# Optimization experiments

Hardware: AMD Instinct MI355X
Metric: run time of the kernel (lower is better)

The kernel has to match this reference:

```python
import jax, jax.numpy as jnp
import numpy as np

B, C, H, W = 1, 256, 96, 96
C8 = C // 8
N = H * W


def setup_inputs() -> dict:
    key = jax.random.key(0)
    ks = jax.random.split(key, 12)
    inp = {
        "x": jax.random.normal(ks[0], (B, C, H, W), jnp.float32),
        "x_encoder": jax.random.normal(ks[1], (B, C, H, W), jnp.float32),
        # 1x1 conv params (weight stored as [out, in] matrices)
        "q_w": jax.random.normal(ks[2], (C8, C), jnp.float32) * 0.05,
        "q_b": jax.random.normal(ks[3], (C8,), jnp.float32) * 0.05,
        "k_w": jax.random.normal(ks[4], (C8, C), jnp.float32) * 0.05,
        "k_b": jax.random.normal(ks[5], (C8,), jnp.float32) * 0.05,
        "v_w": jax.random.normal(ks[6], (C, C), jnp.float32) * 0.05,
        "v_b": jax.random.normal(ks[7], (C,), jnp.float32) * 0.05,
        # positional bias parameters
        "h_pos": jax.random.normal(ks[8], (1, C8, H, 1), jnp.float32),
        "w_pos": jax.random.normal(ks[9], (1, C8, 1, W), jnp.float32),
        # gamma is zero-init in the module; use a random scalar for a non-trivial test
        "gamma": jax.random.normal(ks[10], (1,), jnp.float32),
    }
    return inp


def reference(x, x_encoder, q_w, q_b, k_w, k_b, v_w, v_b, h_pos, w_pos, gamma):
    b, c, h, w = x.shape
    n = h * w
    c8 = q_w.shape[0]
    # 1x1 convs == per-pixel linear maps
    query = (jnp.einsum('bchw,oc->bohw', x, q_w) + q_b[None, :, None, None])
    query = query.reshape(b, c8, n).transpose(0, 2, 1)            # [B, N, C8]
    key = (jnp.einsum('bchw,oc->bohw', x_encoder, k_w) + k_b[None, :, None, None])
    key = key.reshape(b, c8, n)                                   # [B, C8, N]
    # positional bias: broadcast-add then flatten, same as (height+width).view
    pos = (h_pos + w_pos).reshape(1, c8, n)                       # [1, C8, N]
    # energy = Q K^T + Q pos  ==  Q (K + pos)
    energy = jnp.einsum('bnc,bcm->bnm', query, key + pos)         # [B, N, N]
    attention = jax.nn.softmax(energy, axis=-1)
    value = (jnp.einsum('bchw,oc->bohw', x_encoder, v_w) + v_b[None, :, None, None])
    value = value.reshape(b, c, n)                                # [B, C, N]
    out = jnp.einsum('bcm,bnm->bcn', value, attention)            # [B, C, N]
    out = out.reshape(b, c, w, h)  # matches torch .view(B, C, W, H)
    return gamma * out + x
```

## Files before the change

### kernel.cpp

```cpp
#include <hip/hip_runtime.h>
#include <hip/hip_bf16.h>

#define NN 9216
#define CC 256
#define LOG2E 1.4426950408889634f

typedef __attribute__((ext_vector_type(8))) short short8;
typedef __attribute__((ext_vector_type(16))) float floatx16;
typedef __attribute__((ext_vector_type(4))) float floatx4;
typedef __attribute__((ext_vector_type(4))) unsigned short ushortx4;

#if __has_builtin(__builtin_amdgcn_exp2f)
#define fexp2 __builtin_amdgcn_exp2f
#else
#define fexp2 exp2f
#endif

__device__ __forceinline__ unsigned short f2bf(float f) {
    unsigned u = __float_as_uint(f);
    u = u + 0x7fffu + ((u >> 16) & 1u);
    return (unsigned short)(u >> 16);
}
__device__ __forceinline__ float bf2f(unsigned short s) {
    return __uint_as_float(((unsigned)s) << 16);
}
__device__ __forceinline__ unsigned pack2bf(float a, float b) {
    union { __hip_bfloat162 h; unsigned u; } cv;
    cv.h = __float22bfloat162_rn(make_float2(a, b));
    return cv.u;
}
__device__ __forceinline__ floatx16 mfma_bf16(short8 a, short8 b, floatx16 c) {
    return __builtin_amdgcn_mfma_f32_32x32x16_bf16(a, b, c, 0, 0, 0);
}

__global__ __launch_bounds__(256) void prep(
    const float* __restrict__ x, const float* __restrict__ xe,
    short* __restrict__ XBhi, short* __restrict__ XBlo,
    short* __restrict__ EBhi, short* __restrict__ EBlo)
{
    int t = threadIdx.x;
    const float* in = blockIdx.y ? xe : x;
    short* Dhi = blockIdx.y ? EBhi : XBhi;
    short* Dlo = blockIdx.y ? EBlo : XBlo;
    int tl = t & 31, sub = t >> 5;
    int nt = blockIdx.x >> 2, q4 = blockIdx.x & 3;
    int sub2 = q4 * 8 + sub;
    int kb_ = sub2 >> 1, hl = sub2 & 1;
    int n = nt * 32 + tl;
    int c0 = kb_ * 16 + hl * 8;
    union { unsigned short us[8]; short8 v8; } hi, lo;
#pragma unroll
    for (int j = 0; j < 8; ++j) {
        float val = in[(size_t)(c0 + j) * NN + n];
        unsigned short hb = f2bf(val);
        hi.us[j] = hb;
        lo.us[j] = f2bf(val - bf2f(hb));
    }
    size_t off = (((size_t)nt * 16 + kb_) * 64 + hl * 32 + tl) * 8;
    *(short8*)(Dhi + off) = hi.v8;
    *(short8*)(Dlo + off) = lo.v8;
}

__global__ __launch_bounds__(256) void wprep(
    const float* __restrict__ qw, const float* __restrict__ kw,
    const float* __restrict__ vw,
    short* __restrict__ WAhi, short* __restrict__ WAlo)
{
    int g = blockIdx.x * 256 + threadIdx.x;
    int lane = g & 63, kb_ = (g >> 6) & 15, ot = g >> 10;
    int o = lane & 31, half = lane >> 5;
    int c0 = kb_ * 16 + half * 8;
    const float* wsrc;
    int orow;
    float scale = 1.f;
    if (ot == 0) { wsrc = qw; orow = o; scale = LOG2E; }
    else if (ot == 1) { wsrc = kw; orow = o; }
    else { wsrc = vw; orow = (ot - 2) * 32 + o; }
    union { unsigned short us[8]; short8 v8; } hi, lo;
#pragma unroll
    for (int j = 0; j < 8; ++j) {
        float val = wsrc[(size_t)orow * 256 + c0 + j] * scale;
        unsigned short hb = f2bf(val);
        hi.us[j] = hb;
        lo.us[j] = f2bf(val - bf2f(hb));
    }
    size_t off = (((size_t)ot * 16 + kb_) * 64 + lane) * 8;
    *(short8*)(WAhi + off) = hi.v8;
    *(short8*)(WAlo + off) = lo.v8;
}

__global__ __launch_bounds__(256) void gemm_all(
    const short* __restrict__ XBhi, const short* __restrict__ XBlo,
    const short* __restrict__ EBhi, const short* __restrict__ EBlo,
    const short* __restrict__ WAhi, const short* __restrict__ WAlo,
    const float* __restrict__ qb, const float* __restrict__ kb,
    const float* __restrict__ hpos, const float* __restrict__ wpos,
    const float* __restrict__ vb,
    short* __restrict__ Qhi, short* __restrict__ Qlo,
    short* __restrict__ KP2, short* __restrict__ VF)
{
    __shared__ float lds[4][1024];
    int t = threadIdx.x;
    int wv = t >> 6, lane = t & 63, ln = lane & 31, h = lane >> 5;
    int nt = blockIdx.x * 2 + (wv & 1);
    int tile = blockIdx.y * 2 + (wv >> 1);

    const short* Bhi = (tile == 0 ? XBhi : EBhi) + (size_t)nt * 8192 + lane * 8;
    const short* Blo = (tile == 0 ? XBlo : EBlo) + (size_t)nt * 8192 + lane * 8;
    const short* Ahi = WAhi + (size_t)tile * 8192 + lane * 8;
    const short* Alo = WAlo + (size_t)tile * 8192 + lane * 8;

    floatx16 D;
#pragma unroll
    for (int r = 0; r < 16; ++r) D[r] = 0.f;
#pragma unroll
    for (int k = 0; k < 16; ++k) {
        short8 bh = *(const short8*)(Bhi + k * 512);
        short8 bl = *(const short8*)(Blo + k * 512);
        short8 ah = *(const short8*)(Ahi + k * 512);
        short8 al = *(const short8*)(Alo + k * 512);
        D = mfma_bf16(ah, bh, D);
        D = mfma_bf16(ah, bl, D);
        D = mfma_bf16(al, bh, D);
    }

    float* L = lds[wv];
#pragma unroll
    for (int r = 0; r < 16; ++r) {
        int row = (r & 3) + 8 * (r >> 2) + 4 * h;
        L[row * 32 + ((ln + row) & 31)] = D[r];
    }
    __syncthreads();

    if (tile == 0) {
        int n = nt * 32 + ln;
#pragma unroll
        for (int it = 0; it < 2; ++it) {
            int j0 = it * 16 + h * 8;
            union { unsigned short us[8]; short8 v8; } qh_, ql_;
#pragma unroll
            for (int jj = 0; jj < 8; ++jj) {
                int row = j0 + jj;
                float d = L[row * 32 + ((ln + row) & 31)] + qb[row] * LOG2E;
                unsigned short hb = f2bf(d);
                qh_.us[jj] = hb;
                ql_.us[jj] = f2bf(d - bf2f(hb));
            }
            *(short8*)(Qhi + (size_t)n * 32 + j0) = qh_.v8;
            *(short8*)(Qlo + (size_t)n * 32 + j0) = ql_.v8;
        }
    } else if (tile == 1) {
        int n = nt * 32 + ln;
        int hh = ((n >> 5) * 683) >> 11;
        int ww = n - hh * 96;
#pragma unroll
        for (int it = 0; it < 2; ++it) {
            int jb0 = it * 16 + h * 8;
            union { unsigned short us[8]; short8 v8; } o;
#pragma unroll
            for (int jj = 0; jj < 8; ++jj) {
                int row = jb0 + jj;
                float d = L[row * 32 + ((ln + row) & 31)]
                        + kb[row] + hpos[row * 96 + hh] + wpos[row * 96 + ww];
                o.us[jj] = f2bf(d);
            }
            *(short8*)(KP2 + (size_t)nt * 1024 + it * 512 + h * 256 + ln * 8) = o.v8;
        }
    } else {
        int cc = tile - 2;
        float bias = vb[cc * 32 + ln];
#pragma unroll
        for (int it = 0; it < 2; ++it) {
            union { unsigned short us[8]; short8 v8; } o;
#pragma unroll
            for (int ee = 0; ee < 8; ++ee) {
                int ml = it * 16 + h * 8 + ee;
                float d = L[ln * 32 + ((ml + ln) & 31)];
                o.us[ee] = f2bf(d + bias);
            }
            *(short8*)(VF + ((size_t)(nt * 2 + it) * 8 + cc) * 512 + lane * 8) = o.v8;
        }
    }
}

#define FSTEP(AH0, AH1, M0) do {                                                      \
    const size_t mo_ = (size_t)(M0) * 256;                                            \
    short8 va0 = *(const short8*)(Vb + mo_);                                          \
    short8 va1 = *(const short8*)(Vb + mo_ + 512);                                    \
    short8 va2 = *(const short8*)(Vb + mo_ + 1024);                                   \
    short8 va3 = *(const short8*)(Vb + mo_ + 1536);                                   \
    floatx16 S = {0.f,0.f,0.f,0.f,0.f,0.f,0.f,0.f,0.f,0.f,0.f,0.f,0.f,0.f,0.f,0.f};  \
    S = mfma_bf16(AH0, qf00, S);                                                      \
    S = mfma_bf16(AH0, qf01, S);                                                      \
    S = mfma_bf16(AH1, qf10, S);                                                      \
    S = mfma_bf16(AH1, qf11, S);                                                      \
    short8 va4 = *(const short8*)(Vb + mo_ + 2048);                                   \
    short8 va5 = *(const short8*)(Vb + mo_ + 2560);                                   \
    short8 va6 = *(const short8*)(Vb + mo_ + 3072);                                   \
    short8 va7 = *(const short8*)(Vb + mo_ + 3584);                                   \
    float ps = 0.f;                                                                   \
    _Pragma("unroll") for (int r = 0; r < 16; ++r) { S[r] = fexp2(S[r]); ps += S[r]; } \
    ps += __shfl_xor(ps, 32); l_run += ps;                                            \
    unsigned w0 = pack2bf(S[0], S[1]),  w1 = pack2bf(S[2], S[3]);                     \
    unsigned w2 = pack2bf(S[4], S[5]),  w3 = pack2bf(S[6], S[7]);                     \
    unsigned w4 = pack2bf(S[8], S[9]),  w5 = pack2bf(S[10], S[11]);                   \
    unsigned w6 = pack2bf(S[12], S[13]), w7 = pack2bf(S[14], S[15]);                  \
    {   unsigned p0 = h ? w0 : w2, p1 = h ? w1 : w3;                                  \
        unsigned e0 = (unsigned)__shfl_xor((int)p0, 32);                              \
        unsigned e1 = (unsigned)__shfl_xor((int)p1, 32);                              \
        union { unsigned u[4]; short8 v; } pf;                                        \
        pf.u[0] = h ? e0 : w0; pf.u[1] = h ? e1 : w1;                                 \
        pf.u[2] = h ? w2 : e0; pf.u[3] = h ? w3 : e1;                                 \
        O0 = mfma_bf16(va0, pf.v, O0); O1 = mfma_bf16(va1, pf.v, O1);                 \
        O2 = mfma_bf16(va2, pf.v, O2); O3 = mfma_bf16(va3, pf.v, O3);                 \
        O4 = mfma_bf16(va4, pf.v, O4); O5 = mfma_bf16(va5, pf.v, O5);                 \
        O6 = mfma_bf16(va6, pf.v, O6); O7 = mfma_bf16(va7, pf.v, O7); }               \
    short8 vb0 = *(const short8*)(Vb + mo_ + 4096);                                   \
    short8 vb1 = *(const short8*)(Vb + mo_ + 4608);                                   \
    short8 vb2 = *(const short8*)(Vb + mo_ + 5120);                                   \
    short8 vb3 = *(const short8*)(Vb + mo_ + 5632);                                   \
    short8 vb4 = *(const short8*)(Vb + mo_ + 6144);                                   \
    short8 vb5 = *(const short8*)(Vb + mo_ + 6656);                                   \
    short8 vb6 = *(const short8*)(Vb + mo_ + 7168);                                   \
    short8 vb7 = *(const short8*)(Vb + mo_ + 7680);                                   \
    {   unsigned p0 = h ? w4 : w6, p1 = h ? w5 : w7;                                  \
        unsigned e0 = (unsigned)__shfl_xor((int)p0, 32);                              \
        unsigned e1 = (unsigned)__shfl_xor((int)p1, 32);                              \
        union { unsigned u[4]; short8 v; } pf;                                        \
        pf.u[0] = h ? e0 : w4; pf.u[1] = h ? e1 : w5;                                 \
        pf.u[2] = h ? w6 : e0; pf.u[3] = h ? w7 : e1;                                 \
        O0 = mfma_bf16(vb0, pf.v, O0); O1 = mfma_bf16(vb1, pf.v, O1);                 \
        O2 = mfma_bf16(vb2, pf.v, O2); O3 = mfma_bf16(vb3, pf.v, O3);                 \
        O4 = mfma_bf16(vb4, pf.v, O4); O5 = mfma_bf16(vb5, pf.v, O5);                 \
        O6 = mfma_bf16(vb6, pf.v, O6); O7 = mfma_bf16(vb7, pf.v, O7); }               \
} while (0)

#define OGW(G, OG) { _Pragma("unroll") for (int r = 0; r < 16; ++r) { \
    int row = 32*(G) + (r & 3) + 8*(r >> 2) + 4*h;                    \
    Opart[obase + (size_t)row * NN + n0 + ln] = f2bf(OG[r]); } }

__global__ __launch_bounds__(128, 2) void flash(
    const short* __restrict__ Qhi, const short* __restrict__ Qlo,
    const short* __restrict__ KP2, const short* __restrict__ VT2,
    unsigned short* __restrict__ Opart, float* __restrict__ Lpart)
{
    int t = threadIdx.x;
    int wv = t >> 6;
    int lane = t & 63;
    int ln = lane & 31;
    int h = lane >> 5;
    int nt = blockIdx.x >> 2, mq = blockIdx.x & 3;
    int n0 = nt * 64 + wv * 32;
    int mstart = mq * 2304;

    int qoff = (n0 + ln) * 32 + h * 8;
    short8 qf00 = *(const short8*)(Qhi + qoff);
    short8 qf10 = *(const short8*)(Qhi + qoff + 16);
    short8 qf01 = *(const short8*)(Qlo + qoff);
    short8 qf11 = *(const short8*)(Qlo + qoff + 16);

    const short* Vb  = VT2 + (size_t)mstart * 256 + (size_t)lane * 8;
    const short* KPb = KP2 + (size_t)mstart * 32 + (size_t)lane * 8;

    floatx16 O0, O1, O2, O3, O4, O5, O6, O7;
#pragma unroll
    for (int r = 0; r < 16; ++r) {
        O0[r] = 0.f; O1[r] = 0.f; O2[r] = 0.f; O3[r] = 0.f;
        O4[r] = 0.f; O5[r] = 0.f; O6[r] = 0.f; O7[r] = 0.f;
    }
    float l_run = 0.f;

    short8 ahA0 = *(const short8*)(KPb);
    short8 ahA1 = *(const short8*)(KPb + 512);
    short8 ahB0, ahB1;

    for (int sp = 0; sp < 36; ++sp) {
        int m0 = sp * 64;
        ahB0 = *(const short8*)(KPb + (size_t)(m0 + 32) * 32);
        ahB1 = *(const short8*)(KPb + (size_t)(m0 + 32) * 32 + 512);
        FSTEP(ahA0, ahA1, m0);
        int nm = (sp < 35) ? (m0 + 64) : 0;
        ahA0 = *(const short8*)(KPb + (size_t)nm * 32);
        ahA1 = *(const short8*)(KPb + (size_t)nm * 32 + 512);
        FSTEP(ahB0, ahB1, m0 + 32);
    }

    if (lane < 32) Lpart[mq * NN + n0 + ln] = l_run;
    size_t obase = (size_t)mq * ((size_t)CC * NN);
    OGW(0,O0) OGW(1,O1) OGW(2,O2) OGW(3,O3) OGW(4,O4) OGW(5,O5) OGW(6,O6) OGW(7,O7)
}

__global__ __launch_bounds__(256) void stats(
    const float* __restrict__ Lpart, const float* __restrict__ gamma,
    float* __restrict__ W)
{
    int n = blockIdx.x * 256 + threadIdx.x;
    float L = Lpart[n] + Lpart[NN + n] + Lpart[2 * NN + n] + Lpart[3 * NN + n];
    W[n] = gamma[0] / L;
}

__global__ __launch_bounds__(256) void combine(
    const unsigned short* __restrict__ Opart, const float* __restrict__ W,
    const float* __restrict__ x, float* __restrict__ out)
{
    int i = blockIdx.x * 256 + threadIdx.x;
    int flat = i * 4;
    int n = flat % NN;
    floatx4 acc = *(const floatx4*)&x[flat];
    floatx4 w = *(const floatx4*)&W[n];
    float s0 = 0.f, s1 = 0.f, s2 = 0.f, s3 = 0.f;
#pragma unroll
    for (int q = 0; q < 4; ++q) {
        ushortx4 o = *(const ushortx4*)(Opart + (size_t)q * ((size_t)CC * NN) + flat);
        s0 += bf2f(o[0]); s1 += bf2f(o[1]); s2 += bf2f(o[2]); s3 += bf2f(o[3]);
    }
    acc[0] += s0 * w[0]; acc[1] += s1 * w[1]; acc[2] += s2 * w[2]; acc[3] += s3 * w[3];
    *(floatx4*)&out[flat] = acc;
}

extern "C" void kernel_launch(void* const* d_in, const int* in_sizes, int n_in,
                              void* d_out, int out_size, void* d_ws, size_t ws_size,
                              hipStream_t stream) {
    const float* x  = (const float*)d_in[0];
    const float* xe = (const float*)d_in[1];
    const float* qw = (const float*)d_in[2];
    const float* qb = (const float*)d_in[3];
    const float* kw = (const float*)d_in[4];
    const float* kb = (const float*)d_in[5];
    const float* vw = (const float*)d_in[6];
    const float* vb = (const float*)d_in[7];
    const float* hp = (const float*)d_in[8];
    const float* wp = (const float*)d_in[9];
    const float* gm = (const float*)d_in[10];

    char* ws = (char*)d_ws;
    short* Qhi  = (short*)(ws + 0);
    short* Qlo  = (short*)(ws + 589824);
    short* KP2  = (short*)(ws + 1179648);
    short* WAhi = (short*)(ws + 1769472);
    short* WAlo = (short*)(ws + 1933312);
    short* VF   = (short*)(ws + 2097152);
    unsigned short* Opart = (unsigned short*)(ws + 6815744);
    short* XBhi = (short*)(ws + 6815744);
    short* XBlo = (short*)(ws + 11534336);
    short* EBhi = (short*)(ws + 16252928);
    short* EBlo = (short*)(ws + 20971520);
    float* Lpart = (float*)(ws + 25837568);
    float* W     = (float*)(ws + 25985024);

    prep<<<dim3(1152, 2), dim3(256), 0, stream>>>(x, xe, XBhi, XBlo, EBhi, EBlo);
    wprep<<<dim3(40), dim3(256), 0, stream>>>(qw, kw, vw, WAhi, WAlo);
    gemm_all<<<dim3(144, 5), dim3(256), 0, stream>>>(
        XBhi, XBlo, EBhi, EBlo, WAhi, WAlo, qb, kb, hp, wp, vb, Qhi, Qlo, KP2, VF);
    flash<<<dim3(576), dim3(128), 0, stream>>>(Qhi, Qlo, KP2, VF, Opart, Lpart);
    stats<<<dim3(36), dim3(256), 0, stream>>>(Lpart, gm, W);
    combine<<<dim3(2304), dim3(256), 0, stream>>>(Opart, W, x, (float*)d_out);
}
```

Baseline: 112.2 us.

## Split flash key range into eight parts when workspace allows; fold stats into combine

The flash attention kernel now takes the key-split factor as a runtime parameter. It uses 8 partitions instead of 4 when the workspace is large enough, which raises the grid from 576 to 1152 blocks so more of the GPU's compute units are busy. The separate stats kernel is removed and the combine kernel sums the partial softmax denominators itself, saving one launch. The cost is twice the partial-output traffic (bf16 partials written and read back) and a combine loop that is no longer unrolled.

```diff
diff --git a/kernel.cpp b/kernel.cpp
--- a/kernel.cpp
+++ b/kernel.cpp
@@ -236,22 +236,23 @@
 } while (0)
 
 #define OGW(G, OG) { _Pragma("unroll") for (int r = 0; r < 16; ++r) { \
-    int row = 32*(G) + (r & 3) + 8*(r >> 2) + 4*h;                    \
+    int row = 32*(G) + (r & 3) + 8 * (r >> 2) + 4 * h;                \
     Opart[obase + (size_t)row * NN + n0 + ln] = f2bf(OG[r]); } }
 
 __global__ __launch_bounds__(128, 2) void flash(
     const short* __restrict__ Qhi, const short* __restrict__ Qlo,
     const short* __restrict__ KP2, const short* __restrict__ VT2,
-    unsigned short* __restrict__ Opart, float* __restrict__ Lpart)
+    unsigned short* __restrict__ Opart, float* __restrict__ Lpart,
+    int mqmask, int mshift, int mlen)
 {
     int t = threadIdx.x;
     int wv = t >> 6;
     int lane = t & 63;
     int ln = lane & 31;
     int h = lane >> 5;
-    int nt = blockIdx.x >> 2, mq = blockIdx.x & 3;
+    int nt = blockIdx.x >> mshift, mq = blockIdx.x & mqmask;
     int n0 = nt * 64 + wv * 32;
-    int mstart = mq * 2304;
+    int mstart = mq * mlen;
 
     int qoff = (n0 + ln) * 32 + h * 8;
     short8 qf00 = *(const short8*)(Qhi + qoff);
@@ -274,12 +275,13 @@
     short8 ahA1 = *(const short8*)(KPb + 512);
     short8 ahB0, ahB1;
 
-    for (int sp = 0; sp < 36; ++sp) {
+    int nsp = mlen >> 6;
+    for (int sp = 0; sp < nsp; ++sp) {
         int m0 = sp * 64;
         ahB0 = *(const short8*)(KPb + (size_t)(m0 + 32) * 32);
         ahB1 = *(const short8*)(KPb + (size_t)(m0 + 32) * 32 + 512);
         FSTEP(ahA0, ahA1, m0);
-        int nm = (sp < 35) ? (m0 + 64) : 0;
+        int nm = (sp < nsp - 1) ? (m0 + 64) : 0;
         ahA0 = *(const short8*)(KPb + (size_t)nm * 32);
         ahA1 = *(const short8*)(KPb + (size_t)nm * 32 + 512);
         FSTEP(ahB0, ahB1, m0 + 32);
@@ -287,34 +289,32 @@
 
     if (lane < 32) Lpart[mq * NN + n0 + ln] = l_run;
     size_t obase = (size_t)mq * ((size_t)CC * NN);
-    OGW(0,O0) OGW(1,O1) OGW(2,O2) OGW(3,O3) OGW(4,O4) OGW(5,O5) OGW(6,O6) OGW(7,O7)
-}
-
-__global__ __launch_bounds__(256) void stats(
-    const float* __restrict__ Lpart, const float* __restrict__ gamma,
-    float* __restrict__ W)
-{
-    int n = blockIdx.x * 256 + threadIdx.x;
-    float L = Lpart[n] + Lpart[NN + n] + Lpart[2 * NN + n] + Lpart[3 * NN + n];
-    W[n] = gamma[0] / L;
+    OGW(0, O0) OGW(1, O1) OGW(2, O2) OGW(3, O3)
+    OGW(4, O4) OGW(5, O5) OGW(6, O6) OGW(7, O7)
 }
 
 __global__ __launch_bounds__(256) void combine(
-    const unsigned short* __restrict__ Opart, const float* __restrict__ W,
-    const float* __restrict__ x, float* __restrict__ out)
+    const unsigned short* __restrict__ Opart, const float* __restrict__ Lpart,
+    const float* __restrict__ gamma, const float* __restrict__ x,
+    float* __restrict__ out, int nparts)
 {
     int i = blockIdx.x * 256 + threadIdx.x;
     int flat = i * 4;
     int n = flat % NN;
     floatx4 acc = *(const floatx4*)&x[flat];
-    floatx4 w = *(const floatx4*)&W[n];
+    float Ls0 = 0.f, Ls1 = 0.f, Ls2 = 0.f, Ls3 = 0.f;
     float s0 = 0.f, s1 = 0.f, s2 = 0.f, s3 = 0.f;
-#pragma unroll
-    for (int q = 0; q < 4; ++q) {
+    for (int q = 0; q < nparts; ++q) {
+        floatx4 Lq = *(const floatx4*)&Lpart[q * NN + n];
+        Ls0 += Lq[0]; Ls1 += Lq[1]; Ls2 += Lq[2]; Ls3 += Lq[3];
         ushortx4 o = *(const ushortx4*)(Opart + (size_t)q * ((size_t)CC * NN) + flat);
         s0 += bf2f(o[0]); s1 += bf2f(o[1]); s2 += bf2f(o[2]); s3 += bf2f(o[3]);
     }
-    acc[0] += s0 * w[0]; acc[1] += s1 * w[1]; acc[2] += s2 * w[2]; acc[3] += s3 * w[3];
+    float g = gamma[0];
+    acc[0] += s0 * (g / Ls0);
+    acc[1] += s1 * (g / Ls1);
+    acc[2] += s2 * (g / Ls2);
+    acc[3] += s3 * (g / Ls3);
     *(floatx4*)&out[flat] = acc;
 }
 
@@ -340,19 +340,25 @@
     short* WAhi = (short*)(ws + 1769472);
     short* WAlo = (short*)(ws + 1933312);
     short* VF   = (short*)(ws + 2097152);
-    unsigned short* Opart = (unsigned short*)(ws + 6815744);
-    short* XBhi = (short*)(ws + 6815744);
-    short* XBlo = (short*)(ws + 11534336);
-    short* EBhi = (short*)(ws + 16252928);
-    short* EBlo = (short*)(ws + 20971520);
-    float* Lpart = (float*)(ws + 25837568);
-    float* W     = (float*)(ws + 25985024);
+
+    const size_t OPART_OFF = 6815744;
+    const size_t PART_BYTES = (size_t)CC * NN * 2;
+    int nparts = 4, mshift = 2;
+    size_t need8 = OPART_OFF + 8 * PART_BYTES + (size_t)8 * NN * 4;
+    if (ws_size >= need8) { nparts = 8; mshift = 3; }
+    unsigned short* Opart = (unsigned short*)(ws + OPART_OFF);
+    float* Lpart = (float*)(ws + OPART_OFF + (size_t)nparts * PART_BYTES);
+
+    short* XBhi = (short*)(ws + OPART_OFF);
+    short* XBlo = (short*)(ws + OPART_OFF + 4718592);
+    short* EBhi = (short*)(ws + OPART_OFF + 2 * 4718592);
+    short* EBlo = (short*)(ws + OPART_OFF + 3 * 4718592);
 
     prep<<<dim3(1152, 2), dim3(256), 0, stream>>>(x, xe, XBhi, XBlo, EBhi, EBlo);
     wprep<<<dim3(40), dim3(256), 0, stream>>>(qw, kw, vw, WAhi, WAlo);
     gemm_all<<<dim3(144, 5), dim3(256), 0, stream>>>(
         XBhi, XBlo, EBhi, EBlo, WAhi, WAlo, qb, kb, hp, wp, vb, Qhi, Qlo, KP2, VF);
-    flash<<<dim3(576), dim3(128), 0, stream>>>(Qhi, Qlo, KP2, VF, Opart, Lpart);
-    stats<<<dim3(36), dim3(256), 0, stream>>>(Lpart, gm, W);
-    combine<<<dim3(2304), dim3(256), 0, stream>>>(Opart, W, x, (float*)d_out);
-}
+    flash<<<dim3(144 * nparts), dim3(128), 0, stream>>>(
+        Qhi, Qlo, KP2, VF, Opart, Lpart, nparts - 1, mshift, NN / nparts);
+    combine<<<dim3(2304), dim3(256), 0, stream>>>(Opart, Lpart, gm, x, (float*)d_out, nparts);
+}
```

Result: no change. 114.1 us (+1.7%).
